# Performance work log

Measured on AMD Instinct MI355X. Metric: run time of the kernel, lower is better.

Reference implementation:

```python
import jax, jax.numpy as jnp
import numpy as np

EPS = 1e-6

def _ln(x):
    # LayerNorm without affine, biased variance (matches torch default)
    m = jnp.mean(x, axis=-1, keepdims=True)
    v = jnp.var(x, axis=-1, keepdims=True)
    return (x - m) / jnp.sqrt(v + EPS)

def setup_inputs() -> dict:
    key = jax.random.key(0)
    ks = jax.random.split(key, 12)
    B, N, C = 8, 4096, 768
    H = C * 4
    s = 0.02
    return {
        "x":   jax.random.normal(ks[0], (B, N, C), dtype=jnp.float32),
        "Wq":  jax.random.normal(ks[1], (C, C), dtype=jnp.float32) * s,
        "bq":  jnp.zeros((C,), dtype=jnp.float32),
        "Wkv": jax.random.normal(ks[2], (C, 2 * C), dtype=jnp.float32) * s,
        "bkv": jnp.zeros((2 * C,), dtype=jnp.float32),
        "Wo":  jax.random.normal(ks[3], (C, C), dtype=jnp.float32) * s,
        "bo":  jnp.zeros((C,), dtype=jnp.float32),
        "W1":  jax.random.normal(ks[4], (C, H), dtype=jnp.float32) * s,
        "b1":  jnp.zeros((H,), dtype=jnp.float32),
        "W2":  jax.random.normal(ks[5], (H, C), dtype=jnp.float32) * s,
        "b2":  jnp.zeros((C,), dtype=jnp.float32),
    }

def reference(x, Wq, bq, Wkv, bkv, Wo, bo, W1, b1, W2, b2):
    B, N, C = x.shape
    h = 16
    d = C // h
    scale = d ** -0.5

    xn = _ln(x)                          # norm1 over full sequence
    past = xn[:, :-1, :]                 # [B, N-1, C]
    cur = xn[:, -1, :]                   # [B, C]

    q = (cur @ Wq + bq).reshape(B, h, 1, d)                 # [B,h,1,d]
    kv = past @ Wkv + bkv                                   # [B,N-1,2C]
    k, v = jnp.split(kv, 2, axis=-1)
    k = k.reshape(B, N - 1, h, d).transpose(0, 2, 1, 3)     # [B,h,N-1,d]
    v = v.reshape(B, N - 1, h, d).transpose(0, 2, 1, 3)

    sim = jnp.einsum('bhqd,bhkd->bhqk', q, k) * scale       # [B,h,1,N-1]
    attn = jax.nn.softmax(sim, axis=-1)
    out = jnp.einsum('bhqk,bhkd->bhqd', attn, v)            # [B,h,1,d]
    out = out.transpose(0, 2, 1, 3).reshape(B, C)           # [B,C]
    out = out @ Wo + bo

    last = x[:, -1, :] + out                                # attn residual
    mlp = jax.nn.gelu(_ln(last) @ W1 + b1, approximate=True) @ W2 + b2
    last = last + mlp                                       # mlp residual

    return x.at[:, -1, :].set(last)
```

## Files before the change

kernel.cpp:

```cpp
#include <hip/hip_runtime.h>

#define B_ 8
#define N_ 4096
#define C_ 768
#define NP_ 4095
#define H_ 16
#define D_ 48
#define HID_ 3072
#define SCALE 0.14433756729740643f

typedef unsigned short u16;
typedef unsigned int u32;
typedef __attribute__((ext_vector_type(4))) float f32x4;
typedef __attribute__((ext_vector_type(8))) short short8;

__device__ __forceinline__ u32 f2bf_bits(float f){
  union { float f; u32 i; } v; v.f = f;
  return (v.i + 0x7fffu + ((v.i >> 16) & 1u)) >> 16;
}
__device__ __forceinline__ u16 f2bf(float f){ return (u16)f2bf_bits(f); }
__device__ __forceinline__ float bf2f(u16 u){
  union { u32 i; float f; } v; v.i = ((u32)u) << 16; return v.f;
}
__device__ __forceinline__ u32 pack2(float a, float b){
  return f2bf_bits(a) | (f2bf_bits(b) << 16);
}

__global__ __launch_bounds__(256) void k_q(const float* __restrict__ x,
    const float* __restrict__ Wq, const float* __restrict__ bq,
    float* __restrict__ qv, float* __restrict__ zbase)
{
  int b = blockIdx.y, t = threadIdx.x;
  int j0 = blockIdx.x*32;
  {
    int gid = (b*24 + blockIdx.x)*256 + t;
    for (int u = gid; u < 98560; u += 49152) zbase[u] = 0.f;
  }
  __shared__ float xs[C_];
  __shared__ float red[32][9];
  __shared__ float redA[4], redB[4];
  const float* xr = x + ((size_t)b*N_ + NP_)*C_;
  float v0 = xr[t], v1 = xr[t+256], v2 = xr[t+512];
  float s = v0+v1+v2, q = v0*v0+v1*v1+v2*v2;
  #pragma unroll
  for (int off=32; off; off>>=1){ s += __shfl_xor(s,off); q += __shfl_xor(q,off); }
  int w = t>>6, l = t&63;
  if (l==0){ redA[w]=s; redB[w]=q; }
  __syncthreads();
  s = redA[0]+redA[1]+redA[2]+redA[3];
  q = redB[0]+redB[1]+redB[2]+redB[3];
  float mean = s*(1.f/C_), var = q*(1.f/C_) - mean*mean;
  float rstd = rsqrtf(var + 1e-6f);
  xs[t] = (v0-mean)*rstd; xs[t+256] = (v1-mean)*rstd; xs[t+512] = (v2-mean)*rstd;
  __syncthreads();
  int jl = t&31, part = t>>5;
  const float* wp = Wq + (size_t)(part*96)*C_ + j0 + jl;
  const float* xp = xs + part*96;
  float acc = 0.f;
  #pragma unroll 8
  for (int c=0;c<96;c++) acc += xp[c]*wp[(size_t)c*C_];
  red[jl][part] = acc;
  __syncthreads();
  if (part==0){
    float a = bq[j0+jl];
    #pragma unroll
    for (int p=0;p<8;p++) a += red[jl][p];
    qv[(size_t)b*C_ + j0 + jl] = a;
  }
}

__global__ __launch_bounds__(256) void k_qw(const float* __restrict__ qv,
    const float* __restrict__ Wkv, u16* __restrict__ qWb)
{
  int b = blockIdx.y, t = threadIdx.x;
  int c0 = blockIdx.x*16;
  __shared__ float qs[C_];
  for (int u=t; u<C_; u+=256) qs[u] = qv[(size_t)b*C_+u];
  __syncthreads();
  int h = t&15, cl = t>>4;
  int c = c0 + cl;
  const float* wp = Wkv + (size_t)c*(2*C_) + h*D_;
  const float* qh = qs + h*D_;
  float acc = 0.f;
  #pragma unroll
  for (int d=0; d<D_; d++) acc += qh[d]*wp[d];
  qWb[((size_t)b*H_ + h)*C_ + c] = f2bf(acc);
}

__global__ __launch_bounds__(256) void k_pre(const float* __restrict__ x,
    const u16* __restrict__ qWb, float* __restrict__ outp,
    u16* __restrict__ wrsT, float* __restrict__ denom, float* __restrict__ corr)
{
  int b = blockIdx.y;
  int tid = threadIdx.x;
  int w = tid>>6, l = tid&63;
  int kblk = blockIdx.x*16;
  __shared__ float smean[4][16], ssq[4][16];
  __shared__ float2 stl[16];
  __shared__ float part[4][16][17];
  const size_t xb = (size_t)b*N_*C_;

  int r = l & 15;
  int row = kblk + r;
  int cb = w*192 + ((l>>4)<<3);
  const float* xp = x + xb + (size_t)row*C_ + cb;
  float* op = outp + xb + (size_t)row*C_ + cb;

  float4 g[12];
  float s = 0.f, q = 0.f;
  #pragma unroll
  for (int s2=0; s2<6; ++s2){
    float4 a0 = *(const float4*)(xp + s2*32);
    float4 a1 = *(const float4*)(xp + s2*32 + 4);
    g[2*s2] = a0; g[2*s2+1] = a1;
    *(float4*)(op + s2*32)     = a0;
    *(float4*)(op + s2*32 + 4) = a1;
    s += a0.x+a0.y+a0.z+a0.w + a1.x+a1.y+a1.z+a1.w;
    q += a0.x*a0.x+a0.y*a0.y+a0.z*a0.z+a0.w*a0.w
       + a1.x*a1.x+a1.y*a1.y+a1.z*a1.z+a1.w*a1.w;
  }
  s += __shfl_xor(s,16); q += __shfl_xor(q,16);
  s += __shfl_xor(s,32); q += __shfl_xor(q,32);
  if (l < 16){ smean[w][l] = s; ssq[w][l] = q; }
  __syncthreads();
  float fs = smean[0][r]+smean[1][r]+smean[2][r]+smean[3][r];
  float fq = ssq[0][r]+ssq[1][r]+ssq[2][r]+ssq[3][r];
  float mean = fs*(1.f/C_), var = fq*(1.f/C_) - mean*mean;
  float rstd = rsqrtf(var + 1e-6f);
  if (tid < 16) stl[tid] = make_float2(mean, rstd);

  const u16* brb = qWb + ((size_t)b*H_ + r)*C_ + cb;
  f32x4 acc = {0.f,0.f,0.f,0.f};
  #pragma unroll
  for (int s2=0;s2<6;s2++){
    float4 a0 = g[2*s2], a1 = g[2*s2+1];
    union{uint4 u; short8 v;} A, Bf;
    A.u.x = pack2((a0.x-mean)*rstd, (a0.y-mean)*rstd);
    A.u.y = pack2((a0.z-mean)*rstd, (a0.w-mean)*rstd);
    A.u.z = pack2((a1.x-mean)*rstd, (a1.y-mean)*rstd);
    A.u.w = pack2((a1.z-mean)*rstd, (a1.w-mean)*rstd);
    Bf.u = *(const uint4*)(brb + s2*32);
    acc = __builtin_amdgcn_mfma_f32_16x16x32_bf16(A.v, Bf.v, acc, 0,0,0);
  }
  {
    int mb = (l>>4)*4, n = l&15;
    #pragma unroll
    for (int r4=0;r4<4;r4++) part[w][mb+r4][n] = acc[r4];
  }
  __syncthreads();

  {
    int m = tid>>4, n = tid&15;
    float sim = part[0][m][n] + part[1][m][n] + part[2][m][n] + part[3][m][n];
    int kt = kblk + m;
    float2 ms = stl[m];
    float wv = (kt < NP_) ? __expf(sim*SCALE) : 0.f;
    u16 wb = f2bf(wv * ms.y);
    wrsT[((size_t)b*H_ + n)*N_ + kt] = wb;
    part[0][m][n] = wv;
    part[1][m][n] = bf2f(wb) * ms.x;
  }
  __syncthreads();
  if (tid < 16){
    float ds = 0.f, cs = 0.f;
    #pragma unroll
    for (int m=0;m<16;m++){ ds += part[0][m][tid]; cs += part[1][m][tid]; }
    atomicAdd(denom + (size_t)b*H_ + tid, ds);
    atomicAdd(corr  + (size_t)b*H_ + tid, cs);
  }
}

__global__ __launch_bounds__(256) void k_ctx2(const float* __restrict__ x,
    const u16* __restrict__ wrsT, float* __restrict__ ctx)
{
  int b = blockIdx.y;
  int cg = blockIdx.x % 12;
  int ks = blockIdx.x / 12;
  int tid = threadIdx.x;
  int w = tid>>6, l = tid&63;
  int ctile = cg*64 + w*16;
  int k0 = ks*512;
  const size_t xb = (size_t)b*N_*C_;
  const u16* ap = wrsT + ((size_t)b*H_ + (l&15))*N_ + k0 + (l>>4)*8;
  const float* bp = x + xb + (size_t)(k0 + (l>>4)*8)*C_ + ctile + (l&15);
  f32x4 acc = {0.f,0.f,0.f,0.f};
  for (int s=0;s<16;s++){
    union{uint4 u; short8 v;} A, Bf;
    A.u = *(const uint4*)(ap + s*32);
    const float* bq2 = bp + (size_t)s*32*C_;
    float x0 = bq2[0];
    float x1 = bq2[(size_t)1*C_];
    float x2 = bq2[(size_t)2*C_];
    float x3 = bq2[(size_t)3*C_];
    float x4 = bq2[(size_t)4*C_];
    float x5 = bq2[(size_t)5*C_];
    float x6 = bq2[(size_t)6*C_];
    float x7 = bq2[(size_t)7*C_];
    uint4 nb;
    nb.x = pack2(x0,x1); nb.y = pack2(x2,x3);
    nb.z = pack2(x4,x5); nb.w = pack2(x6,x7);
    Bf.u = nb;
    acc = __builtin_amdgcn_mfma_f32_16x16x32_bf16(A.v, Bf.v, acc, 0,0,0);
  }
  int cc = ctile + (l&15);
  float* cb = ctx + (size_t)b*H_*C_;
  #pragma unroll
  for (int r=0;r<4;r++){
    int h = (l>>4)*4 + r;
    atomicAdd(cb + h*C_ + cc, acc[r]);
  }
}

__global__ __launch_bounds__(256) void k_v(const float* __restrict__ ctx,
    const float* __restrict__ denom, const float* __restrict__ corr,
    const float* __restrict__ Wkv, const float* __restrict__ bkv,
    float* __restrict__ oat)
{
  int b = blockIdx.y, t = threadIdx.x;
  int t0 = blockIdx.x*32;
  int h0 = t0/D_;
  int h1 = (t0+31)/D_; if (h1 > H_-1) h1 = H_-1;
  __shared__ float cn[2][C_];
  __shared__ float red[32][9];
  float inv0 = 1.f/denom[(size_t)b*H_+h0];
  float inv1 = 1.f/denom[(size_t)b*H_+h1];
  float cr0 = corr[(size_t)b*H_+h0];
  float cr1 = corr[(size_t)b*H_+h1];
  for (int u=t; u<C_; u+=256){
    cn[0][u] = (ctx[((size_t)b*H_+h0)*C_+u] - cr0)*inv0;
    cn[1][u] = (ctx[((size_t)b*H_+h1)*C_+u] - cr1)*inv1;
  }
  __syncthreads();
  int jl = t&31, part = t>>5;
  int tt = t0 + jl;
  int hi = (tt/D_) - h0;
  const float* wp = Wkv + (size_t)(part*96)*(2*C_) + C_ + tt;
  const float* cp = cn[hi] + part*96;
  float acc = 0.f;
  #pragma unroll 8
  for (int c=0;c<96;c++) acc += cp[c]*wp[(size_t)c*(2*C_)];
  red[jl][part] = acc;
  __syncthreads();
  if (part==0){
    float a = bkv[C_ + tt];
    #pragma unroll
    for (int p=0;p<8;p++) a += red[jl][p];
    oat[(size_t)b*C_ + tt] = a;
  }
}

__global__ __launch_bounds__(256) void k_o(const float* __restrict__ x,
    const float* __restrict__ oat, const float* __restrict__ Wo,
    const float* __restrict__ bo, float* __restrict__ lastb)
{
  int b = blockIdx.y, t = threadIdx.x;
  int t0 = blockIdx.x*32;
  __shared__ float xs[C_];
  __shared__ float red[32][9];
  for (int u=t; u<C_; u+=256) xs[u] = oat[(size_t)b*C_+u];
  __syncthreads();
  int jl = t&31, part = t>>5;
  int tt = t0 + jl;
  const float* wp = Wo + (size_t)(part*96)*C_ + tt;
  const float* xp = xs + part*96;
  float acc = 0.f;
  #pragma unroll 8
  for (int c=0;c<96;c++) acc += xp[c]*wp[(size_t)c*C_];
  red[jl][part] = acc;
  __syncthreads();
  if (part==0){
    float a = bo[tt];
    #pragma unroll
    for (int p=0;p<8;p++) a += red[jl][p];
    lastb[(size_t)b*C_ + tt] = x[((size_t)b*N_ + NP_)*C_ + tt] + a;
  }
}

__global__ __launch_bounds__(256) void k_mlp1(const float* __restrict__ lastb,
    const float* __restrict__ W1, const float* __restrict__ b1,
    float* __restrict__ hid)
{
  int t = threadIdx.x;
  int j0 = blockIdx.x*16;
  __shared__ float xs[B_][C_];
  __shared__ float red[16][16][8];
  {
    int bb = t>>5, sub = t&31;
    const float* xr = lastb + (size_t)bb*C_;
    float s=0.f, q=0.f;
    #pragma unroll
    for (int j=0;j<24;j++){ float v = xr[sub+32*j]; s += v; q += v*v; }
    #pragma unroll
    for (int off=1; off<32; off<<=1){ s += __shfl_xor(s,off); q += __shfl_xor(q,off); }
    float mean = s*(1.f/C_), var = q*(1.f/C_) - mean*mean;
    float rstd = rsqrtf(var + 1e-6f);
    #pragma unroll
    for (int j=0;j<24;j++){ xs[bb][sub+32*j] = (xr[sub+32*j]-mean)*rstd; }
  }
  __syncthreads();
  int jl = t&15, part = t>>4;
  const float* wp = W1 + (size_t)(part*48)*HID_ + j0 + jl;
  float acc[B_];
  #pragma unroll
  for (int bb=0;bb<B_;bb++) acc[bb]=0.f;
  for (int c=0;c<48;c++){
    float wv = wp[(size_t)c*HID_];
    int cc = part*48 + c;
    #pragma unroll
    for (int bb=0;bb<B_;bb++) acc[bb] += xs[bb][cc]*wv;
  }
  #pragma unroll
  for (int bb=0;bb<B_;bb++) red[jl][part][bb] = acc[bb];
  __syncthreads();
  if (t < 128){
    int jl2 = t&15, bb = t>>4;
    float a = b1[j0+jl2];
    #pragma unroll
    for (int p=0;p<16;p++) a += red[jl2][p][bb];
    float t3 = a + 0.044715f*a*a*a;
    float g = 0.5f*a*(1.f + tanhf(0.7978845608f*t3));
    hid[(size_t)bb*HID_ + j0 + jl2] = g;
  }
}

__global__ __launch_bounds__(256) void k_mlp2(const float* __restrict__ hid,
    const float* __restrict__ W2, const float* __restrict__ b2,
    const float* __restrict__ lastb, float* __restrict__ outp)
{
  int t = threadIdx.x;
  int c0 = blockIdx.x*8;
  __shared__ float red[8][32][8];
  int ccl = t&7, part = t>>3;
  const float* wp = W2 + (size_t)(part*96)*C_ + c0 + ccl;
  float acc[B_];
  #pragma unroll
  for (int bb=0;bb<B_;bb++) acc[bb]=0.f;
  for (int j=0;j<96;j++){
    float wv = wp[(size_t)j*C_];
    int jj = part*96 + j;
    #pragma unroll
    for (int bb=0;bb<B_;bb++) acc[bb] += hid[(size_t)bb*HID_ + jj]*wv;
  }
  #pragma unroll
  for (int bb=0;bb<B_;bb++) red[ccl][part][bb] = acc[bb];
  __syncthreads();
  if (t < 64){
    int cc2 = t&7, bb = t>>3;
    float a = 0.f;
    #pragma unroll
    for (int p=0;p<32;p++) a += red[cc2][p][bb];
    int cc = c0 + cc2;
    a += b2[cc] + lastb[(size_t)bb*C_ + cc];
    outp[((size_t)bb*N_ + NP_)*C_ + cc] = a;
  }
}

extern "C" void kernel_launch(void* const* d_in, const int* in_sizes, int n_in,
                              void* d_out, int out_size, void* d_ws, size_t ws_size,
                              hipStream_t stream)
{
  (void)in_sizes; (void)n_in; (void)out_size; (void)ws_size;
  const float* x   = (const float*)d_in[0];
  const float* Wq  = (const float*)d_in[1];
  const float* bq  = (const float*)d_in[2];
  const float* Wkv = (const float*)d_in[3];
  const float* bkv = (const float*)d_in[4];
  const float* Wo  = (const float*)d_in[5];
  const float* bo  = (const float*)d_in[6];
  const float* W1  = (const float*)d_in[7];
  const float* b1  = (const float*)d_in[8];
  const float* W2  = (const float*)d_in[9];
  const float* b2  = (const float*)d_in[10];
  float* outp = (float*)d_out;
  float* ws = (float*)d_ws;
  float* ctx    = ws;
  float* denom  = ctx + 98304;
  float* corr   = denom + 128;
  float* qv     = corr + 128;
  float* oat    = qv + 6144;
  float* lastb  = oat + 6144;
  float* hid    = lastb + 6144;
  u16*   qWb    = (u16*)(hid + 24576);
  u16*   wrsT   = (u16*)(hid + 24576 + 49152);

  hipLaunchKernelGGL(k_q,    dim3(24,B_), dim3(256), 0, stream, x, Wq, bq, qv, ctx);
  hipLaunchKernelGGL(k_qw,   dim3(48,B_), dim3(256), 0, stream, qv, Wkv, qWb);
  hipLaunchKernelGGL(k_pre,  dim3(256,B_), dim3(256), 0, stream, x, qWb, outp, wrsT, denom, corr);
  hipLaunchKernelGGL(k_ctx2, dim3(96,B_), dim3(256), 0, stream, x, wrsT, ctx);
  hipLaunchKernelGGL(k_v,    dim3(24,B_), dim3(256), 0, stream, ctx, denom, corr, Wkv, bkv, oat);
  hipLaunchKernelGGL(k_o,    dim3(24,B_), dim3(256), 0, stream, x, oat, Wo, bo, lastb);
  hipLaunchKernelGGL(k_mlp1, dim3(192), dim3(256), 0, stream, lastb, W1, b1, hid);
  hipLaunchKernelGGL(k_mlp2, dim3(96), dim3(256), 0, stream, hid, W2, b2, lastb, outp);
}
```

Before: 109.7 us.

## Process two 16-row tiles per k_pre block with nontemporal output copies

k_pre now handles 32 rows per block in two stages, issuing all x loads up front for both tiles and hoisting the qWb B-fragment loads out of the loop so they are reused across both tiles. The copy of x into the output uses nontemporal stores so it does not displace x from cache before k_ctx2 reads it. Per-block atomics for denom/corr are halved by accumulating across both stages. The grid is halved to 128 blocks per batch, which raises register pressure from 24 float4 registers and reduces block count, possibly lowering occupancy.

```diff
diff --git a/kernel.cpp b/kernel.cpp
--- a/kernel.cpp
+++ b/kernel.cpp
@@ -25,6 +25,10 @@
 __device__ __forceinline__ u32 pack2(float a, float b){
   return f2bf_bits(a) | (f2bf_bits(b) << 16);
 }
+__device__ __forceinline__ void nt_store4(float* p, float4 v){
+  union { float4 h; f32x4 n; } u; u.h = v;
+  __builtin_nontemporal_store(u.n, (f32x4*)p);
+}
 
 __global__ __launch_bounds__(256) void k_q(const float* __restrict__ x,
     const float* __restrict__ Wq, const float* __restrict__ bq,
@@ -94,72 +98,99 @@
   int b = blockIdx.y;
   int tid = threadIdx.x;
   int w = tid>>6, l = tid&63;
-  int kblk = blockIdx.x*16;
+  int kblk = blockIdx.x*32;
   __shared__ float smean[4][16], ssq[4][16];
   __shared__ float2 stl[16];
   __shared__ float part[4][16][17];
   const size_t xb = (size_t)b*N_*C_;
 
   int r = l & 15;
-  int row = kblk + r;
   int cb = w*192 + ((l>>4)<<3);
-  const float* xp = x + xb + (size_t)row*C_ + cb;
-  float* op = outp + xb + (size_t)row*C_ + cb;
-
-  float4 g[12];
-  float s = 0.f, q = 0.f;
-  #pragma unroll
-  for (int s2=0; s2<6; ++s2){
-    float4 a0 = *(const float4*)(xp + s2*32);
-    float4 a1 = *(const float4*)(xp + s2*32 + 4);
-    g[2*s2] = a0; g[2*s2+1] = a1;
-    *(float4*)(op + s2*32)     = a0;
-    *(float4*)(op + s2*32 + 4) = a1;
-    s += a0.x+a0.y+a0.z+a0.w + a1.x+a1.y+a1.z+a1.w;
-    q += a0.x*a0.x+a0.y*a0.y+a0.z*a0.z+a0.w*a0.w
-       + a1.x*a1.x+a1.y*a1.y+a1.z*a1.z+a1.w*a1.w;
-  }
-  s += __shfl_xor(s,16); q += __shfl_xor(q,16);
-  s += __shfl_xor(s,32); q += __shfl_xor(q,32);
-  if (l < 16){ smean[w][l] = s; ssq[w][l] = q; }
-  __syncthreads();
-  float fs = smean[0][r]+smean[1][r]+smean[2][r]+smean[3][r];
-  float fq = ssq[0][r]+ssq[1][r]+ssq[2][r]+ssq[3][r];
-  float mean = fs*(1.f/C_), var = fq*(1.f/C_) - mean*mean;
-  float rstd = rsqrtf(var + 1e-6f);
-  if (tid < 16) stl[tid] = make_float2(mean, rstd);
-
-  const u16* brb = qWb + ((size_t)b*H_ + r)*C_ + cb;
-  f32x4 acc = {0.f,0.f,0.f,0.f};
+
+  uint4 Bf[6];
+  {
+    const u16* brb = qWb + ((size_t)b*H_ + r)*C_ + cb;
+    #pragma unroll
+    for (int s2=0;s2<6;s2++) Bf[s2] = *(const uint4*)(brb + s2*32);
+  }
+
+  const float* xp0 = x + xb + (size_t)(kblk + r)*C_ + cb;
+  const float* xp1 = xp0 + (size_t)16*C_;
+  float* op0 = outp + xb + (size_t)(kblk + r)*C_ + cb;
+  float* op1 = op0 + (size_t)16*C_;
+
+  float4 g0[12], g1[12];
   #pragma unroll
   for (int s2=0;s2<6;s2++){
-    float4 a0 = g[2*s2], a1 = g[2*s2+1];
-    union{uint4 u; short8 v;} A, Bf;
-    A.u.x = pack2((a0.x-mean)*rstd, (a0.y-mean)*rstd);
-    A.u.y = pack2((a0.z-mean)*rstd, (a0.w-mean)*rstd);
-    A.u.z = pack2((a1.x-mean)*rstd, (a1.y-mean)*rstd);
-    A.u.w = pack2((a1.z-mean)*rstd, (a1.w-mean)*rstd);
-    Bf.u = *(const uint4*)(brb + s2*32);
-    acc = __builtin_amdgcn_mfma_f32_16x16x32_bf16(A.v, Bf.v, acc, 0,0,0);
-  }
-  {
-    int mb = (l>>4)*4, n = l&15;
-    #pragma unroll
-    for (int r4=0;r4<4;r4++) part[w][mb+r4][n] = acc[r4];
-  }
-  __syncthreads();
-
-  {
-    int m = tid>>4, n = tid&15;
-    float sim = part[0][m][n] + part[1][m][n] + part[2][m][n] + part[3][m][n];
-    int kt = kblk + m;
-    float2 ms = stl[m];
-    float wv = (kt < NP_) ? __expf(sim*SCALE) : 0.f;
-    u16 wb = f2bf(wv * ms.y);
-    wrsT[((size_t)b*H_ + n)*N_ + kt] = wb;
-    part[0][m][n] = wv;
-    part[1][m][n] = bf2f(wb) * ms.x;
-  }
+    g0[2*s2]   = *(const float4*)(xp0 + s2*32);
+    g0[2*s2+1] = *(const float4*)(xp0 + s2*32 + 4);
+  }
+  #pragma unroll
+  for (int s2=0;s2<6;s2++){
+    g1[2*s2]   = *(const float4*)(xp1 + s2*32);
+    g1[2*s2+1] = *(const float4*)(xp1 + s2*32 + 4);
+  }
+
+  float ds_local = 0.f, cs_local = 0.f;
+
+  auto stage = [&](float4 (&g)[12], float* op, int st){
+    #pragma unroll
+    for (int s2=0;s2<6;s2++){
+      nt_store4(op + s2*32,     g[2*s2]);
+      nt_store4(op + s2*32 + 4, g[2*s2+1]);
+    }
+    float s = 0.f, q = 0.f;
+    #pragma unroll
+    for (int j=0;j<12;j++){
+      float4 a = g[j];
+      s += a.x+a.y+a.z+a.w;
+      q += a.x*a.x+a.y*a.y+a.z*a.z+a.w*a.w;
+    }
+    s += __shfl_xor(s,16); q += __shfl_xor(q,16);
+    s += __shfl_xor(s,32); q += __shfl_xor(q,32);
+    if (l < 16){ smean[w][l] = s; ssq[w][l] = q; }
+    __syncthreads();
+    float fs = smean[0][r]+smean[1][r]+smean[2][r]+smean[3][r];
+    float fq = ssq[0][r]+ssq[1][r]+ssq[2][r]+ssq[3][r];
+    float mean = fs*(1.f/C_), var = fq*(1.f/C_) - mean*mean;
+    float rstd = rsqrtf(var + 1e-6f);
+    if (tid < 16) stl[tid] = make_float2(mean, rstd);
+    f32x4 acc = {0.f,0.f,0.f,0.f};
+    #pragma unroll
+    for (int s2=0;s2<6;s2++){
+      float4 a0 = g[2*s2], a1 = g[2*s2+1];
+      union{uint4 u; short8 v;} A, B2;
+      A.u.x = pack2((a0.x-mean)*rstd, (a0.y-mean)*rstd);
+      A.u.y = pack2((a0.z-mean)*rstd, (a0.w-mean)*rstd);
+      A.u.z = pack2((a1.x-mean)*rstd, (a1.y-mean)*rstd);
+      A.u.w = pack2((a1.z-mean)*rstd, (a1.w-mean)*rstd);
+      B2.u = Bf[s2];
+      acc = __builtin_amdgcn_mfma_f32_16x16x32_bf16(A.v, B2.v, acc, 0,0,0);
+    }
+    {
+      int mb = (l>>4)*4, n = l&15;
+      #pragma unroll
+      for (int r4=0;r4<4;r4++) part[w][mb+r4][n] = acc[r4];
+    }
+    __syncthreads();
+    {
+      int m = tid>>4, n = tid&15;
+      float sim = part[0][m][n] + part[1][m][n] + part[2][m][n] + part[3][m][n];
+      int kt = kblk + st*16 + m;
+      float2 ms = stl[m];
+      float wv = (kt < NP_) ? __expf(sim*SCALE) : 0.f;
+      u16 wb = f2bf(wv * ms.y);
+      wrsT[((size_t)b*H_ + n)*N_ + kt] = wb;
+      ds_local += wv;
+      cs_local += bf2f(wb) * ms.x;
+    }
+    __syncthreads();
+  };
+  stage(g0, op0, 0);
+  stage(g1, op1, 1);
+
+  part[0][tid>>4][tid&15] = ds_local;
+  part[1][tid>>4][tid&15] = cs_local;
   __syncthreads();
   if (tid < 16){
     float ds = 0.f, cs = 0.f;
@@ -385,7 +416,7 @@
 
   hipLaunchKernelGGL(k_q,    dim3(24,B_), dim3(256), 0, stream, x, Wq, bq, qv, ctx);
   hipLaunchKernelGGL(k_qw,   dim3(48,B_), dim3(256), 0, stream, qv, Wkv, qWb);
-  hipLaunchKernelGGL(k_pre,  dim3(256,B_), dim3(256), 0, stream, x, qWb, outp, wrsT, denom, corr);
+  hipLaunchKernelGGL(k_pre,  dim3(128,B_), dim3(256), 0, stream, x, qWb, outp, wrsT, denom, corr);
   hipLaunchKernelGGL(k_ctx2, dim3(96,B_), dim3(256), 0, stream, x, wrsT, ctx);
   hipLaunchKernelGGL(k_v,    dim3(24,B_), dim3(256), 0, stream, ctx, denom, corr, Wkv, bkv, oat);
   hipLaunchKernelGGL(k_o,    dim3(24,B_), dim3(256), 0, stream, x, oat, Wo, bo, lastb);
```

Result: slower. 113.6 us (+3.6%).
